# Kernel tuning notes

Hardware: AMD Instinct MI355X
Metric: run time of the kernel (lower is better)

## Reference

```python
import math
import jax, jax.numpy as jnp
import numpy as np

B, S, D = 4, 4096, 1024

def setup_inputs() -> dict:
    key = jax.random.key(0)
    ks = jax.random.split(key, 4)
    scale = 1.0 / math.sqrt(D)
    return {
        "x": jax.random.normal(ks[0], (B, S, D), dtype=jnp.float32),
        "Wq": jax.random.normal(ks[1], (D, D), dtype=jnp.float32) * scale,
        "bq": jnp.zeros((D,), dtype=jnp.float32),
        "Wk": jax.random.normal(ks[2], (D, D), dtype=jnp.float32) * scale,
        "bk": jnp.zeros((D,), dtype=jnp.float32),
        "Wv": jax.random.normal(ks[3], (D, D), dtype=jnp.float32) * scale,
        "bv": jnp.zeros((D,), dtype=jnp.float32),
    }

def reference(x, Wq, bq, Wk, bk, Wv, bv):
    # Linear layers (torch nn.Linear: x @ W.T + b)
    Q = jnp.einsum('bsd,ed->bse', x, Wq) + bq  # [B,S,D]
    K = jnp.einsum('bsd,ed->bse', x, Wk) + bk
    V = jnp.einsum('bsd,ed->bse', x, Wv) + bv
    # Full (non-flash) attention, scaled by sqrt(hidden_dim) as in source
    scores = jnp.einsum('bqd,bkd->bqk', Q, K) / jnp.sqrt(jnp.float32(Q.shape[-1]))
    attn = jax.nn.softmax(scores, axis=-1)  # [B,S,S]
    return jnp.einsum('bqk,bkd->bqd', attn, V)
```

## Files before the change

kernel.cpp:

```cpp
#include <hip/hip_runtime.h>
#include <hip/hip_bf16.h>
#include <stdint.h>


typedef __attribute__((ext_vector_type(4))) float f32x4;
typedef __attribute__((ext_vector_type(8))) short s16x8;
typedef __attribute__((ext_vector_type(4))) unsigned short u16x4;
typedef unsigned int u32;
typedef unsigned short u16;

__device__ __forceinline__ u16 f2b(float f) {
  u32 u = __float_as_uint(f);
  u = (u + 0x7FFFu + ((u >> 16) & 1u)) >> 16;
  return (u16)u;
}
__device__ __forceinline__ float b2f(u16 h) {
  return __uint_as_float(((u32)h) << 16);
}

__device__ __forceinline__ void gload_lds16(const void* g, void* l) {
  __builtin_amdgcn_global_load_lds(
      (const __attribute__((address_space(1))) void*)(const void*)g,
      (__attribute__((address_space(3))) void*)(void*)l, 16, 0, 0);
}

#define BARRIER() asm volatile("s_barrier" ::: "memory")
#define WAITLGKM0() asm volatile("s_waitcnt lgkmcnt(0)" ::: "memory")
#define WAITVM(N) asm volatile("s_waitcnt vmcnt(" #N ")" ::: "memory")

__global__ __launch_bounds__(256) void k_cvt(const float* __restrict__ in,
                                             u16* __restrict__ out, int n4) {
  int i = blockIdx.x * 256 + threadIdx.x;
  if (i >= n4) return;
  f32x4 f = ((const f32x4*)in)[i];
  u16x4 h;
#pragma unroll
  for (int j = 0; j < 4; ++j) h[j] = f2b(f[j]);
  ((u16x4*)out)[i] = h;
}

template <int MODE>
__global__ __launch_bounds__(512)
void k_gemm256(const u16* __restrict__ A, const u16* __restrict__ B, int lda,
               int ldb, int K, const float* __restrict__ bias,
               const float* __restrict__ biasB, void* __restrict__ Cv, int ldc,
               float scale, size_t az, size_t bz, size_t czb) {
  extern __shared__ __align__(16) u16 lds[];

  A += (size_t)blockIdx.z * az;
  B += (size_t)blockIdx.z * bz;
  char* C = (char*)Cv + (size_t)blockIdx.z * czb;
  const float* bi = (MODE == 0 && blockIdx.z != 0) ? biasB : bias;

  const int gx = gridDim.x;
  const int nwg = gx * gridDim.y;
  const int bid = blockIdx.y * gx + blockIdx.x;
  const int q = nwg >> 3, r = nwg & 7;
  const int xcd = bid & 7, idx = bid >> 3;
  const int tile = (xcd < r ? xcd * (q + 1) : r * (q + 1) + (xcd - r) * q) + idx;
  const int m0 = (tile / gx) * 256;
  const int n0 = (tile % gx) * 256;

  const int tid = threadIdx.x;
  const int lane = tid & 63;
  const int wid = tid >> 6;
  const int wm = wid >> 2;
  const int wn = wid & 3;

  const int srow = lane >> 3;
  const int gcol = (((lane & 7) ^ srow) << 3);
  const int rA = lane & 15;
  const int kq = (lane >> 4) << 3;
  const int xr = (lane & 7) << 3;

#define STAGE_A(h, kt, b)                                                    \
  do {                                                                       \
    _Pragma("unroll") for (int j = 0; j < 2; ++j)                            \
        gload_lds16(A + (size_t)(m0 + (h)*128 + j * 64 + wid * 8 + srow) *   \
                            lda + (kt)*64 + gcol,                            \
                    &lds[(b)*32768 + (h)*8192 + j * 4096 + wid * 512]);      \
  } while (0)
#define STAGE_B(h, kt, b)                                                    \
  do {                                                                       \
    _Pragma("unroll") for (int j = 0; j < 2; ++j)                            \
        gload_lds16(B + (size_t)(n0 + (h)*128 + j * 64 + wid * 8 + srow) *   \
                            ldb + (kt)*64 + gcol,                            \
                    &lds[(b)*32768 + 16384 + (h)*8192 + j * 4096 +           \
                         wid * 512]);                                        \
  } while (0)
#define RD_A(dst, b, sub)                                                    \
  do {                                                                       \
    _Pragma("unroll") for (int mi = 0; mi < 4; ++mi)                         \
        _Pragma("unroll") for (int ks = 0; ks < 2; ++ks)                     \
            dst[mi][ks] = *(const s16x8*)&lds[(b)*32768 +                    \
                (wm * 128 + (sub) + mi * 16 + rA) * 64 +                     \
                ((ks * 32 + kq) ^ xr)];                                      \
  } while (0)
#define RD_B(dst, b, sub)                                                    \
  do {                                                                       \
    _Pragma("unroll") for (int ni = 0; ni < 2; ++ni)                         \
        _Pragma("unroll") for (int ks = 0; ks < 2; ++ks)                     \
            dst[ni][ks] = *(const s16x8*)&lds[(b)*32768 + 16384 +            \
                (wn * 64 + (sub) + ni * 16 + rA) * 64 +                      \
                ((ks * 32 + kq) ^ xr)];                                      \
  } while (0)
#define MM(AF, BF, MO, NO)                                                   \
  do {                                                                       \
    _Pragma("unroll") for (int mi = 0; mi < 4; ++mi)                         \
        _Pragma("unroll") for (int ni = 0; ni < 2; ++ni)                     \
            _Pragma("unroll") for (int ks = 0; ks < 2; ++ks)                 \
                acc[(MO) + mi][(NO) + ni] =                                  \
                    __builtin_amdgcn_mfma_f32_16x16x32_bf16(                 \
                        AF[mi][ks], BF[ni][ks], acc[(MO) + mi][(NO) + ni],   \
                        0, 0, 0);                                            \
  } while (0)

  f32x4 acc[8][4] = {};
  const int NT = K >> 6;

  STAGE_A(0, 0, 0);
  STAGE_A(1, 0, 0);
  STAGE_B(0, 0, 0);
  STAGE_B(1, 0, 0);
  if (NT > 1) {
    STAGE_A(0, 1, 1);
    STAGE_A(1, 1, 1);
    STAGE_B(0, 1, 1);
    STAGE_B(1, 1, 1);
    WAITVM(8);
  } else {
    WAITVM(0);
  }
  BARRIER();

  s16x8 af0[4][2], af1[4][2], bf0[2][2], bf1[2][2];
  for (int t = 0; t < NT; ++t) {
    const int b = t & 1;
    RD_A(af0, b, 0);
    RD_B(bf0, b, 0);
    BARRIER();
    WAITLGKM0();
    __builtin_amdgcn_s_setprio(1);
    MM(af0, bf0, 0, 0);
    __builtin_amdgcn_s_setprio(0);
    BARRIER();
    RD_A(af1, b, 64);
    BARRIER();
    WAITLGKM0();
    __builtin_amdgcn_s_setprio(1);
    MM(af1, bf0, 4, 0);
    __builtin_amdgcn_s_setprio(0);
    BARRIER();
    RD_B(bf1, b, 32);
    if (t + 2 < NT) {
      STAGE_A(0, t + 2, b);
      STAGE_A(1, t + 2, b);
    }
    BARRIER();
    WAITLGKM0();
    __builtin_amdgcn_s_setprio(1);
    MM(af0, bf1, 0, 2);
    __builtin_amdgcn_s_setprio(0);
    BARRIER();
    if (t + 2 < NT) {
      STAGE_B(0, t + 2, b);
      STAGE_B(1, t + 2, b);
    }
    BARRIER();
    __builtin_amdgcn_s_setprio(1);
    MM(af1, bf1, 4, 2);
    __builtin_amdgcn_s_setprio(0);
    if (t + 2 < NT) {
      WAITVM(8);
    } else {
      WAITVM(0);
    }
    BARRIER();
  }

  const int r4 = (lane >> 4) * 4;
#pragma unroll
  for (int nj = 0; nj < 4; ++nj) {
    const int col = n0 + wn * 64 + nj * 16 + (lane & 15);
    float bcol = 0.0f;
    if (MODE == 0) bcol = bi[col];
#pragma unroll
    for (int mi = 0; mi < 8; ++mi) {
#pragma unroll
      for (int rr = 0; rr < 4; ++rr) {
        const int row = m0 + wm * 128 + mi * 16 + r4 + rr;
        float v = acc[mi][nj][rr];
        if (MODE == 0) v += bcol;
        if (MODE == 1) v += bi[row];
        if (MODE == 0 || MODE == 1) {
          ((u16*)C)[(size_t)row * ldc + col] = f2b(v);
        } else if (MODE == 2) {
          ((u16*)C)[(size_t)row * ldc + col] = f2b(v * scale);
        } else {
          ((float*)C)[(size_t)row * ldc + col] = v;
        }
      }
    }
  }
#undef STAGE_A
#undef STAGE_B
#undef RD_A
#undef RD_B
#undef MM
}

__global__ __launch_bounds__(256) void k_softmax(u16* __restrict__ S) {
  __shared__ float redm[4], reds[4];
  const int tid = threadIdx.x;
  const int lane = tid & 63;
  const int wid = tid >> 6;
  u16* sr = S + (size_t)blockIdx.x * 4096;
  s16x8 v[2];
#pragma unroll
  for (int i = 0; i < 2; ++i) v[i] = ((const s16x8*)sr)[i * 256 + tid];
  float f[16];
#pragma unroll
  for (int i = 0; i < 2; ++i)
#pragma unroll
    for (int j = 0; j < 8; ++j) f[i * 8 + j] = b2f((u16)v[i][j]);
  float m = -3.0e38f;
#pragma unroll
  for (int i = 0; i < 16; ++i) m = fmaxf(m, f[i]);
#pragma unroll
  for (int o = 32; o > 0; o >>= 1) m = fmaxf(m, __shfl_xor(m, o, 64));
  if (lane == 0) redm[wid] = m;
  __syncthreads();
  m = fmaxf(fmaxf(redm[0], redm[1]), fmaxf(redm[2], redm[3]));
  float s = 0.f;
#pragma unroll
  for (int i = 0; i < 16; ++i) {
    f[i] = __expf(f[i] - m);
    s += f[i];
  }
#pragma unroll
  for (int o = 32; o > 0; o >>= 1) s += __shfl_xor(s, o, 64);
  if (lane == 0) reds[wid] = s;
  __syncthreads();
  s = reds[0] + reds[1] + reds[2] + reds[3];
  const float inv = 1.0f / s;
#pragma unroll
  for (int i = 0; i < 2; ++i) {
    s16x8 h;
#pragma unroll
    for (int j = 0; j < 8; ++j) h[j] = (short)f2b(f[i * 8 + j] * inv);
    ((s16x8*)sr)[i * 256 + tid] = h;
  }
}

extern "C" void kernel_launch(void* const* d_in, const int* in_sizes, int n_in,
                              void* d_out, int out_size, void* d_ws,
                              size_t ws_size, hipStream_t stream) {
  const float* x = (const float*)d_in[0];
  const float* Wq = (const float*)d_in[1];
  const float* bq = (const float*)d_in[2];
  const float* Wk = (const float*)d_in[3];
  const float* bk = (const float*)d_in[4];
  const float* Wv = (const float*)d_in[5];
  const float* bv = (const float*)d_in[6];
  float* out = (float*)d_out;
  char* ws = (char*)d_ws;

  const size_t MB = 1ull << 20;
  u16* Qb = (u16*)(ws + 0 * MB);
  u16* Kb = (u16*)(ws + 32 * MB);
  u16* VtAll = (u16*)(ws + 64 * MB);
  u16* Xb = (u16*)(ws + 96 * MB);
  u16* Sc = (u16*)(ws + 96 * MB);
  u16* Wqb = (u16*)(ws + 224 * MB);
  u16* Wkb = Wqb + 1048576;
  u16* Wvb = Wqb + 2097152;

  hipFuncSetAttribute((const void*)k_gemm256<0>,
                      hipFuncAttributeMaxDynamicSharedMemorySize, 131072);
  hipFuncSetAttribute((const void*)k_gemm256<1>,
                      hipFuncAttributeMaxDynamicSharedMemorySize, 131072);
  hipFuncSetAttribute((const void*)k_gemm256<2>,
                      hipFuncAttributeMaxDynamicSharedMemorySize, 131072);
  hipFuncSetAttribute((const void*)k_gemm256<3>,
                      hipFuncAttributeMaxDynamicSharedMemorySize, 131072);

  k_cvt<<<16384, 256, 0, stream>>>(x, Xb, 4194304);
  k_cvt<<<1024, 256, 0, stream>>>(Wq, Wqb, 262144);
  k_cvt<<<1024, 256, 0, stream>>>(Wk, Wkb, 262144);
  k_cvt<<<1024, 256, 0, stream>>>(Wv, Wvb, 262144);

  dim3 blk(512);
  const size_t LDSB = 131072;
  k_gemm256<0><<<dim3(4, 64, 2), blk, LDSB, stream>>>(
      Xb, Wqb, 1024, 1024, 1024, bq, bk, Qb, 1024, 1.f, 0, 1048576,
      (size_t)32 * MB);
  k_gemm256<1><<<dim3(64, 4, 1), blk, LDSB, stream>>>(
      Wvb, Xb, 1024, 1024, 1024, bv, nullptr, VtAll, 16384, 1.f, 0, 0, 0);
  k_gemm256<2><<<dim3(16, 16, 4), blk, LDSB, stream>>>(
      Qb, Kb, 1024, 1024, 1024, nullptr, nullptr, Sc, 4096, 0.03125f, 4194304,
      4194304, (size_t)4096 * 4096 * 2);
  k_softmax<<<16384, 256, 0, stream>>>(Sc);
  k_gemm256<3><<<dim3(4, 16, 4), blk, LDSB, stream>>>(
      Sc, VtAll, 4096, 16384, 4096, nullptr, nullptr, out, 1024, 1.f, 16777216,
      4096, (size_t)4096 * 1024 * 4);
}
```

Before: 489.5 us.

## Stage GEMM epilogue through LDS for coalesced vector stores and trim barriers

```diff
diff --git a/kernel.cpp b/kernel.cpp
--- a/kernel.cpp
+++ b/kernel.cpp
@@ -138,14 +138,12 @@
     const int b = t & 1;
     RD_A(af0, b, 0);
     RD_B(bf0, b, 0);
-    BARRIER();
     WAITLGKM0();
     __builtin_amdgcn_s_setprio(1);
     MM(af0, bf0, 0, 0);
     __builtin_amdgcn_s_setprio(0);
     BARRIER();
     RD_A(af1, b, 64);
-    BARRIER();
     WAITLGKM0();
     __builtin_amdgcn_s_setprio(1);
     MM(af1, bf0, 4, 0);
@@ -156,7 +154,6 @@
       STAGE_A(0, t + 2, b);
       STAGE_A(1, t + 2, b);
     }
-    BARRIER();
     WAITLGKM0();
     __builtin_amdgcn_s_setprio(1);
     MM(af0, bf1, 0, 2);
@@ -166,7 +163,6 @@
       STAGE_B(0, t + 2, b);
       STAGE_B(1, t + 2, b);
     }
-    BARRIER();
     __builtin_amdgcn_s_setprio(1);
     MM(af1, bf1, 4, 2);
     __builtin_amdgcn_s_setprio(0);
@@ -178,27 +174,54 @@
     BARRIER();
   }
 
+  float* fl = (float*)lds;
+  const int l15 = lane & 15;
   const int r4 = (lane >> 4) * 4;
-#pragma unroll
-  for (int nj = 0; nj < 4; ++nj) {
-    const int col = n0 + wn * 64 + nj * 16 + (lane & 15);
-    float bcol = 0.0f;
-    if (MODE == 0) bcol = bi[col];
-#pragma unroll
-    for (int mi = 0; mi < 8; ++mi) {
-#pragma unroll
-      for (int rr = 0; rr < 4; ++rr) {
-        const int row = m0 + wm * 128 + mi * 16 + r4 + rr;
-        float v = acc[mi][nj][rr];
-        if (MODE == 0) v += bcol;
-        if (MODE == 1) v += bi[row];
-        if (MODE == 0 || MODE == 1) {
-          ((u16*)C)[(size_t)row * ldc + col] = f2b(v);
-        } else if (MODE == 2) {
-          ((u16*)C)[(size_t)row * ldc + col] = f2b(v * scale);
-        } else {
-          ((float*)C)[(size_t)row * ldc + col] = v;
+  f32x4 bcol4 = {0.f, 0.f, 0.f, 0.f};
+  if (MODE == 0) bcol4 = *(const f32x4*)&bi[n0 + lane * 4];
+#pragma unroll
+  for (int c = 0; c < 4; ++c) {
+    __syncthreads();
+    if (wm == (c >> 1)) {
+      const int mibase = (c & 1) * 4;
+#pragma unroll
+      for (int mi = 0; mi < 4; ++mi) {
+#pragma unroll
+        for (int nj = 0; nj < 4; ++nj) {
+          const int col = wn * 64 + nj * 16 + l15;
+          const int rbase = mi * 16 + r4;
+#pragma unroll
+          for (int rr = 0; rr < 4; ++rr)
+            fl[(rbase + rr) * 260 + col] = acc[mibase + mi][nj][rr];
         }
+      }
+    }
+    __syncthreads();
+#pragma unroll
+    for (int p = 0; p < 8; ++p) {
+      const int rl = p * 8 + wid;
+      const int rowg = m0 + c * 64 + rl;
+      f32x4 v = *(const f32x4*)&fl[rl * 260 + lane * 4];
+      if (MODE == 0) {
+#pragma unroll
+        for (int j = 0; j < 4; ++j) v[j] += bcol4[j];
+        u16x4 h;
+#pragma unroll
+        for (int j = 0; j < 4; ++j) h[j] = f2b(v[j]);
+        ((u16x4*)((u16*)C + (size_t)rowg * ldc + n0))[lane] = h;
+      } else if (MODE == 1) {
+        const float br = bi[rowg];
+        u16x4 h;
+#pragma unroll
+        for (int j = 0; j < 4; ++j) h[j] = f2b(v[j] + br);
+        ((u16x4*)((u16*)C + (size_t)rowg * ldc + n0))[lane] = h;
+      } else if (MODE == 2) {
+        u16x4 h;
+#pragma unroll
+        for (int j = 0; j < 4; ++j) h[j] = f2b(v[j] * scale);
+        ((u16x4*)((u16*)C + (size_t)rowg * ldc + n0))[lane] = h;
+      } else {
+        ((f32x4*)((float*)C + (size_t)rowg * ldc + n0))[lane] = v;
       }
     }
   }
```

Measured after the change: 452.6 us. -7.5%, faster.
